# Kernel optimization log

Measured on AMD Instinct MI355X. Metric: run time of the kernel, lower is better.

## Reference

```python
import jax, jax.numpy as jnp
import numpy as np

N_NODES = 100000


def gcn_conv(x, W, b, src, dst, n):
    """PyG GCNConv: linear transform, symmetric-normalized scatter-add, bias.
    src/dst already include self-loops."""
    h = x @ W                                              # [N, out]
    deg = jax.ops.segment_sum(jnp.ones_like(dst, dtype=h.dtype), dst, num_segments=n)
    dinv = jax.lax.rsqrt(deg)                              # deg >= 1 (self-loops)
    norm = dinv[src] * dinv[dst]                           # [E+N]
    msg = h[src] * norm[:, None]                           # gather + scale
    return jax.ops.segment_sum(msg, dst, num_segments=n) + b


def setup_inputs() -> dict:
    key = jax.random.key(0)
    ks = jax.random.split(key, 8)
    N, E = N_NODES, 1600000
    d_in, d_h, d_out = 128, 128, 64
    x = jax.random.normal(ks[0], (N, d_in), dtype=jnp.float32)
    edge_index = jax.random.randint(ks[1], (2, E), 0, N, dtype=jnp.int64)
    W1 = jax.random.normal(ks[2], (d_in, d_h), dtype=jnp.float32) / np.sqrt(d_in)
    b1 = jnp.zeros((d_h,), dtype=jnp.float32)
    W2 = jax.random.normal(ks[3], (d_h, d_out), dtype=jnp.float32) / np.sqrt(d_h)
    b2 = jnp.zeros((d_out,), dtype=jnp.float32)
    Wfc = jax.random.normal(ks[4], (d_out, 10), dtype=jnp.float32) / np.sqrt(d_out)
    bfc = jnp.zeros((10,), dtype=jnp.float32)
    return {"x": x, "edge_index": edge_index, "W1": W1, "b1": b1,
            "W2": W2, "b2": b2, "Wfc": Wfc, "bfc": bfc}


def reference(x, edge_index, W1, b1, W2, b2, Wfc, bfc):
    n = x.shape[0]
    loops = jnp.arange(n, dtype=edge_index.dtype)
    src = jnp.concatenate([edge_index[0], loops])          # add self-loops
    dst = jnp.concatenate([edge_index[1], loops])
    h = jax.nn.relu(gcn_conv(x, W1, b1, src, dst, n))
    h = jax.nn.relu(gcn_conv(h, W2, b2, src, dst, n))
    return h @ Wfc + bfc                                   # [N, 10]
```

## Files before the change

kernel.cpp:

```cpp
#include <hip/hip_runtime.h>
#include <hip/hip_fp16.h>


static constexpr int NB    = 196;
static constexpr int NPB   = 512;
static constexpr int BCAP  = 9216;
static constexpr int CHUNK = 4096;
static constexpr int PARTA = 524;

typedef _Float16 f16x8 __attribute__((ext_vector_type(8)));
typedef float    f32x4 __attribute__((ext_vector_type(4)));

union HV8 { uint4 u; __half2 h2[4]; __half h[8]; };

__device__ inline void acc8(float* a, const HV8& v, float w) {
#pragma unroll
    for (int i = 0; i < 4; ++i) {
        float2 f = __half22float2(v.h2[i]);
        a[2 * i]     = fmaf(f.x, w, a[2 * i]);
        a[2 * i + 1] = fmaf(f.y, w, a[2 * i + 1]);
    }
}

__device__ inline void gemm1_body(int bid, int tid, _Float16 (*Wt)[136],
                                  const float* __restrict__ X,
                                  const float* __restrict__ W,
                                  __half* __restrict__ Hh, int n) {
    for (int idx = tid; idx < 128 * 128; idx += 256) {
        int k = idx >> 7, c = idx & 127;
        Wt[c][k] = (_Float16)W[idx];
    }
    __syncthreads();
    if (bid * 128 >= n) return;

    int wv = tid >> 6, l = tid & 63;
    int lr = l & 15, lq = l >> 4;
    int rowb = bid * 128 + wv * 32;

    f32x4 acc[2][8];
#pragma unroll
    for (int rt = 0; rt < 2; ++rt)
#pragma unroll
        for (int ct = 0; ct < 8; ++ct) acc[rt][ct] = (f32x4){0.f, 0.f, 0.f, 0.f};

#pragma unroll
    for (int kt = 0; kt < 4; ++kt) {
        int kb = kt * 32 + lq * 8;
        f16x8 af[2];
#pragma unroll
        for (int rt = 0; rt < 2; ++rt) {
            int row = rowb + rt * 16 + lr;
            row = (row < n) ? row : (n - 1);
            const float* xr = X + (size_t)row * 128 + kb;
            float4 xa = *(const float4*)xr;
            float4 xb = *(const float4*)(xr + 4);
            f16x8 a;
            a[0] = (_Float16)xa.x; a[1] = (_Float16)xa.y;
            a[2] = (_Float16)xa.z; a[3] = (_Float16)xa.w;
            a[4] = (_Float16)xb.x; a[5] = (_Float16)xb.y;
            a[6] = (_Float16)xb.z; a[7] = (_Float16)xb.w;
            af[rt] = a;
        }
#pragma unroll
        for (int ct = 0; ct < 8; ++ct) {
            f16x8 bf = *(const f16x8*)&Wt[ct * 16 + lr][kb];
            acc[0][ct] = __builtin_amdgcn_mfma_f32_16x16x32_f16(af[0], bf, acc[0][ct], 0, 0, 0);
            acc[1][ct] = __builtin_amdgcn_mfma_f32_16x16x32_f16(af[1], bf, acc[1][ct], 0, 0, 0);
        }
    }
#pragma unroll
    for (int rt = 0; rt < 2; ++rt)
#pragma unroll
        for (int j = 0; j < 4; ++j) {
            int row = rowb + rt * 16 + lq * 4 + j;
            if (row >= n) continue;
            __half* hr = Hh + (size_t)row * 128 + lr;
#pragma unroll
            for (int ct = 0; ct < 8; ++ct)
                hr[ct * 16] = __float2half(acc[rt][ct][j]);
        }
}

union SharedL1 {
    _Float16 Wt[128][136];
    struct {
        int hist[NB]; int lofs[NB]; int gbase[NB]; int lcur[NB]; int scanv[256];
        unsigned pkbuf[CHUNK]; unsigned short bbuf[CHUNK];
    } s;
};

__global__ __launch_bounds__(256) void k_scat_gemm1(
        const int* __restrict__ src, const int* __restrict__ dst, int E,
        int* __restrict__ gcursor, unsigned* __restrict__ ebuf,
        const float* __restrict__ X, const float* __restrict__ W,
        __half* __restrict__ Hh, int n, int nchunks) {
    __shared__ SharedL1 sh;
    int q = blockIdx.x / 7, r = blockIdx.x % 7;
    int tid = threadIdx.x;
    if (r < 3) {
        int fid = q * 3 + r;
        if (fid >= nchunks) return;
        long long e0 = (long long)fid * CHUNK;
        int m = (int)(((long long)E - e0 < CHUNK) ? (E - e0) : CHUNK);

        for (int i = tid; i < NB; i += 256) sh.s.hist[i] = 0;
        __syncthreads();

        unsigned pk[16]; int bk[16];
#pragma unroll
        for (int i = 0; i < 16; ++i) {
            int idx = i * 256 + tid;
            bool ok = idx < m;
            long long e = e0 + idx;
            int d = ok ? dst[e] : 0;
            int s = ok ? src[e] : 0;
            bk[i] = ok ? (d >> 9) : -1;
            pk[i] = ((unsigned)(d & 511) << 17) | (unsigned)s;
            if (ok) atomicAdd(&sh.s.hist[bk[i]], 1);
        }
        __syncthreads();
        int v = (tid < NB) ? sh.s.hist[tid] : 0;
        sh.s.scanv[tid] = v;
        __syncthreads();
        for (int off = 1; off < 256; off <<= 1) {
            int add = (tid >= off) ? sh.s.scanv[tid - off] : 0;
            __syncthreads();
            sh.s.scanv[tid] += add;
            __syncthreads();
        }
        if (tid < NB) {
            int ex = sh.s.scanv[tid] - v;
            sh.s.lofs[tid] = ex;
            sh.s.lcur[tid] = ex;
            sh.s.gbase[tid] = (v > 0) ? atomicAdd(&gcursor[tid], v) : 0;
        }
        __syncthreads();
#pragma unroll
        for (int i = 0; i < 16; ++i) {
            if (bk[i] >= 0) {
                int slot = atomicAdd(&sh.s.lcur[bk[i]], 1);
                sh.s.pkbuf[slot] = pk[i];
                sh.s.bbuf[slot] = (unsigned short)bk[i];
            }
        }
        __syncthreads();
        for (int i = tid; i < m; i += 256) {
            int b = sh.s.bbuf[i];
            int rel = sh.s.gbase[b] + (i - sh.s.lofs[b]);
            if (rel < BCAP) ebuf[(size_t)b * BCAP + rel] = sh.s.pkbuf[i];
        }
        return;
    }
    int bid = q * 4 + (r - 3);
    if (bid >= PARTA) return;
    gemm1_body(bid, tid, sh.Wt, X, W, Hh, n);
}

union SharedL2 {
    _Float16 Wt[128][136];
    struct { int hist[NPB]; int scanv[256]; int rp[NPB]; int reds[256]; } c;
};

__global__ __launch_bounds__(256) void k_csr_gemm1b(
        const unsigned* __restrict__ ebuf, const int* __restrict__ gcursor,
        int* __restrict__ row_ptr, int* __restrict__ col,
        float* __restrict__ dinv, int N_,
        const float* __restrict__ X, const float* __restrict__ W,
        __half* __restrict__ Hh, int n) {
    __shared__ SharedL2 sh;
    int q = blockIdx.x / 7, r = blockIdx.x % 7;
    int tid = threadIdx.x;
    if (r < 3) {
        int b = q * 3 + r;
        if (b >= NB) return;
        int rv = (tid < NB && tid < b) ? min(gcursor[tid], BCAP) : 0;
        sh.c.reds[tid] = rv;
        __syncthreads();
        for (int off = 128; off > 0; off >>= 1) {
            if (tid < off) sh.c.reds[tid] += sh.c.reds[tid + off];
            __syncthreads();
        }
        int base = sh.c.reds[0];
        __syncthreads();

        for (int i = tid; i < NPB; i += 256) sh.c.hist[i] = 0;
        __syncthreads();
        int cntb = min(gcursor[b], BCAP);
        const unsigned* seg = ebuf + (size_t)b * BCAP;
        for (int i = tid; i < cntb; i += 256)
            atomicAdd(&sh.c.hist[seg[i] >> 17], 1);
        __syncthreads();
        int a0 = sh.c.hist[2 * tid], a1 = sh.c.hist[2 * tid + 1];
        int s = a0 + a1;
        sh.c.scanv[tid] = s;
        __syncthreads();
        for (int off = 1; off < 256; off <<= 1) {
            int add = (tid >= off) ? sh.c.scanv[tid - off] : 0;
            __syncthreads();
            sh.c.scanv[tid] += add;
            __syncthreads();
        }
        int excl = sh.c.scanv[tid] - s;
        sh.c.rp[2 * tid] = excl;
        sh.c.rp[2 * tid + 1] = excl + a0;
        __syncthreads();
        int node0 = b * NPB;
        for (int i = tid; i < NPB; i += 256) {
            int node = node0 + i;
            if (node < N_) {
                row_ptr[node] = base + sh.c.rp[i];
                dinv[node] = rsqrtf((float)(sh.c.hist[i] + 1));
            }
        }
        if (tid == 0 && b == NB - 1) row_ptr[N_] = base + cntb;
        __syncthreads();
        for (int i = tid; i < NPB; i += 256) sh.c.rp[i] += base;
        __syncthreads();
        for (int i = tid; i < cntb; i += 256) {
            unsigned pk = seg[i];
            int pos = atomicAdd(&sh.c.rp[pk >> 17], 1);
            col[pos] = (int)(pk & 0x1FFFFu);
        }
        return;
    }
    int bid = PARTA + q * 4 + (r - 3);
    if (bid * 128 >= n) return;
    gemm1_body(bid, tid, sh.Wt, X, W, Hh, n);
}

__global__ __launch_bounds__(256) void k_gather128(const __half* __restrict__ Hs,
                                                   const float* __restrict__ dinv,
                                                   const int* __restrict__ row_ptr,
                                                   const int* __restrict__ col,
                                                   __half* __restrict__ outh, int n) {
    int wave = threadIdx.x >> 6;
    int lane = threadIdx.x & 63;
    int h = lane >> 5, hl = lane & 31;
    int halfbase = h * 32;
    int qi2 = hl >> 4, ql = hl & 15;
    int node = blockIdx.x * 8 + wave * 2 + h;
    if (node >= n) return;
    int beg = row_ptr[node], end = row_ptr[node + 1];
    int deg = end - beg;

    float acc[8];
#pragma unroll
    for (int v = 0; v < 8; ++v) acc[v] = 0.f;

    for (int base = 0; base < deg; base += 32) {
        int m = deg - base; if (m > 32) m = 32;
        int cl = (hl < m) ? col[beg + base + hl] : 0;
        for (int j = 0; j < m; j += 16) {
            int ss[8]; float ww[8]; HV8 uu[8];
#pragma unroll
            for (int t = 0; t < 8; ++t) {
                int jx = j + t * 2 + qi2;
                bool ok = jx < m;
                ss[t] = __shfl(cl, halfbase + (ok ? jx : j));
                ww[t] = ok ? dinv[ss[t]] : 0.f;
            }
#pragma unroll
            for (int t = 0; t < 8; ++t)
                uu[t].u = *(const uint4*)(Hs + (size_t)ss[t] * 128 + ql * 8);
#pragma unroll
            for (int t = 0; t < 8; ++t) acc8(acc, uu[t], ww[t]);
        }
    }
#pragma unroll
    for (int v = 0; v < 8; ++v) acc[v] += __shfl_xor(acc[v], 16);
    if (qi2 == 0) {
        HV8 su; su.u = *(const uint4*)(Hs + (size_t)node * 128 + ql * 8);
        float dn = dinv[node];
        HV8 o;
#pragma unroll
        for (int i = 0; i < 4; ++i) {
            float2 f = __half22float2(su.h2[i]);
            o.h[2 * i]     = __float2half((acc[2 * i]     + dn * f.x) * dn);
            o.h[2 * i + 1] = __float2half((acc[2 * i + 1] + dn * f.y) * dn);
        }
        *(uint4*)(outh + (size_t)node * 128 + ql * 8) = o.u;
    }
}

__global__ __launch_bounds__(256) void k_gemm2(const __half* __restrict__ A,
                                               const float* __restrict__ W2,
                                               const float* __restrict__ b1,
                                               const float* __restrict__ dinv,
                                               __half* __restrict__ Hh2, int n) {
    __shared__ _Float16 Wt[64][136];
    __shared__ _Float16 b1h[128];
    int tid = threadIdx.x;
    for (int idx = tid; idx < 128 * 64; idx += 256) {
        int k = idx >> 6, c = idx & 63;
        Wt[c][k] = (_Float16)W2[idx];
    }
    if (tid < 128) b1h[tid] = (_Float16)b1[tid];
    __syncthreads();

    int bid = blockIdx.x;
    if (bid * 128 >= n) return;
    int wv = tid >> 6, l = tid & 63;
    int lr = l & 15, lq = l >> 4;
    int rowb = bid * 128 + wv * 32;

    f32x4 acc[2][4];
#pragma unroll
    for (int rt = 0; rt < 2; ++rt)
#pragma unroll
        for (int ct = 0; ct < 4; ++ct) acc[rt][ct] = (f32x4){0.f, 0.f, 0.f, 0.f};

#pragma unroll
    for (int kt = 0; kt < 4; ++kt) {
        int kb = kt * 32 + lq * 8;
        f16x8 bb = *(const f16x8*)&b1h[kb];
        f16x8 af[2];
#pragma unroll
        for (int rt = 0; rt < 2; ++rt) {
            int row = rowb + rt * 16 + lr;
            row = (row < n) ? row : (n - 1);
            f16x8 a = *(const f16x8*)(A + (size_t)row * 128 + kb);
            a = a + bb;
#pragma unroll
            for (int i = 0; i < 8; ++i)
                a[i] = (a[i] > (_Float16)0.f) ? a[i] : (_Float16)0.f;
            af[rt] = a;
        }
#pragma unroll
        for (int ct = 0; ct < 4; ++ct) {
            f16x8 bf = *(const f16x8*)&Wt[ct * 16 + lr][kb];
            acc[0][ct] = __builtin_amdgcn_mfma_f32_16x16x32_f16(af[0], bf, acc[0][ct], 0, 0, 0);
            acc[1][ct] = __builtin_amdgcn_mfma_f32_16x16x32_f16(af[1], bf, acc[1][ct], 0, 0, 0);
        }
    }
#pragma unroll
    for (int rt = 0; rt < 2; ++rt)
#pragma unroll
        for (int j = 0; j < 4; ++j) {
            int row = rowb + rt * 16 + lq * 4 + j;
            if (row >= n) continue;
            float dn = dinv[row];
            __half* hr = Hh2 + (size_t)row * 64 + lr;
#pragma unroll
            for (int ct = 0; ct < 4; ++ct)
                hr[ct * 16] = __float2half(acc[rt][ct][j] * dn);
        }
}

__global__ __launch_bounds__(256) void k_gather_fc(const __half* __restrict__ Hs,
                                                   const float* __restrict__ dinv,
                                                   const int* __restrict__ row_ptr,
                                                   const int* __restrict__ col,
                                                   const float* __restrict__ b2,
                                                   const float* __restrict__ Wfc,
                                                   const float* __restrict__ bfc,
                                                   float* __restrict__ out, int n) {
    int wave = threadIdx.x >> 6;
    int lane = threadIdx.x & 63;
    int h = lane >> 5, hl = lane & 31;
    int halfbase = h * 32;
    int oi2 = hl >> 3, ol = hl & 7;
    float wrowA[10], wrowB[10];
#pragma unroll
    for (int j = 0; j < 10; ++j) {
        wrowA[j] = Wfc[(2 * hl) * 10 + j];
        wrowB[j] = Wfc[(2 * hl + 1) * 10 + j];
    }
    float2 b2v = *(const float2*)(b2 + 2 * hl);

    int node = blockIdx.x * 8 + wave * 2 + h;
    if (node >= n) return;
    int beg = row_ptr[node], end = row_ptr[node + 1];
    int deg = end - beg;

    float acc[8];
#pragma unroll
    for (int v = 0; v < 8; ++v) acc[v] = 0.f;

    for (int base = 0; base < deg; base += 32) {
        int m = deg - base; if (m > 32) m = 32;
        int cl = (hl < m) ? col[beg + base + hl] : 0;
        for (int j = 0; j < m; j += 16) {
            int ss[4]; float ww[4]; HV8 uu[4];
#pragma unroll
            for (int t = 0; t < 4; ++t) {
                int jx = j + t * 4 + oi2;
                bool ok = jx < m;
                ss[t] = __shfl(cl, halfbase + (ok ? jx : j));
                ww[t] = ok ? 1.f : 0.f;
            }
#pragma unroll
            for (int t = 0; t < 4; ++t)
                uu[t].u = *(const uint4*)(Hs + (size_t)ss[t] * 64 + ol * 8);
#pragma unroll
            for (int t = 0; t < 4; ++t) acc8(acc, uu[t], ww[t]);
        }
    }
#pragma unroll
    for (int v = 0; v < 8; ++v) {
        acc[v] += __shfl_xor(acc[v], 16);
        acc[v] += __shfl_xor(acc[v], 8);
    }
    int srcl = halfbase + (hl >> 2);
    float vals[8];
#pragma unroll
    for (int v = 0; v < 8; ++v) vals[v] = __shfl(acc[v], srcl);
    int e = (hl & 3) * 2;
    float aggA = vals[0], aggB = vals[1];
#pragma unroll
    for (int v = 2; v < 8; v += 2) {
        aggA = (e == v) ? vals[v] : aggA;
        aggB = (e == v) ? vals[v + 1] : aggB;
    }
    float2 sf = __half22float2(*(const __half2*)(Hs + (size_t)node * 64 + 2 * hl));
    float dn = dinv[node];
    float vA = fmaxf((aggA + sf.x) * dn + b2v.x, 0.f);
    float vB = fmaxf((aggB + sf.y) * dn + b2v.y, 0.f);
    float p[10];
#pragma unroll
    for (int j = 0; j < 10; ++j) p[j] = vA * wrowA[j] + vB * wrowB[j];
#pragma unroll
    for (int off = 16; off > 0; off >>= 1)
#pragma unroll
        for (int j = 0; j < 10; ++j) p[j] += __shfl_xor(p[j], off);
    if (hl == 0) {
        float* o = out + (size_t)node * 10;
#pragma unroll
        for (int j = 0; j < 10; ++j) o[j] = p[j] + bfc[j];
    }
}

static inline int cdiv(long long a, int b) { return (int)((a + b - 1) / b); }

extern "C" void kernel_launch(void* const* d_in, const int* in_sizes, int n_in,
                              void* d_out, int out_size, void* d_ws, size_t ws_size,
                              hipStream_t stream) {
    const float* x   = (const float*)d_in[0];
    const int*   ei  = (const int*)d_in[1];
    const float* W1  = (const float*)d_in[2];
    const float* b1  = (const float*)d_in[3];
    const float* W2  = (const float*)d_in[4];
    const float* b2  = (const float*)d_in[5];
    const float* Wfc = (const float*)d_in[6];
    const float* bfc = (const float*)d_in[7];
    float* out = (float*)d_out;

    const int N = in_sizes[0] / 128;
    const int E = in_sizes[1] / 2;
    const int* src = ei;
    const int* dst = ei + E;

    char* ws = (char*)d_ws;
    size_t off = 0;
    auto alloc = [&](size_t bytes) { void* p = ws + off; off = (off + bytes + 255) & ~(size_t)255; return p; };
    float*    dinv    = (float*)   alloc((size_t)N * 4);
    int*      row_ptr = (int*)     alloc((size_t)(N + 1) * 4);
    int*      gcursor = (int*)     alloc((size_t)NB * 4);
    unsigned* ebuf    = (unsigned*)alloc((size_t)NB * BCAP * 4);
    int*      col     = (int*)     alloc((size_t)E * 4);
    __half*   Hh1     = (__half*)  alloc((size_t)N * 128 * 2);
    __half*   Ah1     = (__half*)  alloc((size_t)N * 128 * 2);
    __half*   Hh2     = (__half*)  alloc((size_t)N * 64 * 2);

    hipMemsetAsync(gcursor, 0, (size_t)NB * 4, stream);

    const int nchunks = cdiv(E, CHUNK);
    const int groupsL1 = max(cdiv(nchunks, 3), cdiv(PARTA, 4));
    k_scat_gemm1<<<groupsL1 * 7, 256, 0, stream>>>(
        src, dst, E, gcursor, ebuf, x, W1, Hh1, N, nchunks);

    const int gemmTotal = cdiv(N, 128);
    const int groupsL2 = max(cdiv(NB, 3), cdiv(gemmTotal - PARTA, 4));
    k_csr_gemm1b<<<groupsL2 * 7, 256, 0, stream>>>(
        ebuf, gcursor, row_ptr, col, dinv, N, x, W1, Hh1, N);

    k_gather128<<<cdiv(N, 8), 256, 0, stream>>>(Hh1, dinv, row_ptr, col, Ah1, N);

    k_gemm2<<<cdiv(N, 128), 256, 0, stream>>>(Ah1, W2, b1, dinv, Hh2, N);
    k_gather_fc<<<cdiv(N, 8), 256, 0, stream>>>(Hh2, dinv, row_ptr, col,
                                                b2, Wfc, bfc, out, N);
}
```

Measured before the change: 270.4 us.

## Fuse layer-1 aggregation into gemm2 via LDS and accumulate gathers in packed fp16

Merges the layer-1 neighbor gather kernel with the second GEMM. Each 128-node block aggregates its rows into a shared-memory tile, then runs the MFMA GEMM from LDS, so the intermediate Ah1 buffer is never written to or read back from global memory. Both gather loops now accumulate in packed fp16 vectors instead of fp32 scalars, which halves the accumulator registers and the reduction shuffles. The risks are reduced occupancy from the roughly 52KB of LDS, only 782 blocks doing serial 16-pass gathers, and lower precision in the fp16 sums.

Measured after the change: 354.5 us. 1.31x slower.

```diff
diff --git a/kernel.cpp b/kernel.cpp
--- a/kernel.cpp
+++ b/kernel.cpp
@@ -10,17 +10,6 @@
 
 typedef _Float16 f16x8 __attribute__((ext_vector_type(8)));
 typedef float    f32x4 __attribute__((ext_vector_type(4)));
-
-union HV8 { uint4 u; __half2 h2[4]; __half h[8]; };
-
-__device__ inline void acc8(float* a, const HV8& v, float w) {
-#pragma unroll
-    for (int i = 0; i < 4; ++i) {
-        float2 f = __half22float2(v.h2[i]);
-        a[2 * i]     = fmaf(f.x, w, a[2 * i]);
-        a[2 * i + 1] = fmaf(f.y, w, a[2 * i + 1]);
-    }
-}
 
 __device__ inline void gemm1_body(int bid, int tid, _Float16 (*Wt)[136],
                                   const float* __restrict__ X,
@@ -228,86 +217,94 @@
     gemm1_body(bid, tid, sh.Wt, X, W, Hh, n);
 }
 
-__global__ __launch_bounds__(256) void k_gather128(const __half* __restrict__ Hs,
-                                                   const float* __restrict__ dinv,
-                                                   const int* __restrict__ row_ptr,
-                                                   const int* __restrict__ col,
-                                                   __half* __restrict__ outh, int n) {
-    int wave = threadIdx.x >> 6;
-    int lane = threadIdx.x & 63;
-    int h = lane >> 5, hl = lane & 31;
-    int halfbase = h * 32;
-    int qi2 = hl >> 4, ql = hl & 15;
-    int node = blockIdx.x * 8 + wave * 2 + h;
-    if (node >= n) return;
-    int beg = row_ptr[node], end = row_ptr[node + 1];
-    int deg = end - beg;
-
-    float acc[8];
-#pragma unroll
-    for (int v = 0; v < 8; ++v) acc[v] = 0.f;
-
-    for (int base = 0; base < deg; base += 32) {
-        int m = deg - base; if (m > 32) m = 32;
-        int cl = (hl < m) ? col[beg + base + hl] : 0;
-        for (int j = 0; j < m; j += 16) {
-            int ss[8]; float ww[8]; HV8 uu[8];
-#pragma unroll
-            for (int t = 0; t < 8; ++t) {
-                int jx = j + t * 2 + qi2;
-                bool ok = jx < m;
-                ss[t] = __shfl(cl, halfbase + (ok ? jx : j));
-                ww[t] = ok ? dinv[ss[t]] : 0.f;
-            }
-#pragma unroll
-            for (int t = 0; t < 8; ++t)
-                uu[t].u = *(const uint4*)(Hs + (size_t)ss[t] * 128 + ql * 8);
-#pragma unroll
-            for (int t = 0; t < 8; ++t) acc8(acc, uu[t], ww[t]);
-        }
-    }
-#pragma unroll
-    for (int v = 0; v < 8; ++v) acc[v] += __shfl_xor(acc[v], 16);
-    if (qi2 == 0) {
-        HV8 su; su.u = *(const uint4*)(Hs + (size_t)node * 128 + ql * 8);
-        float dn = dinv[node];
-        HV8 o;
-#pragma unroll
-        for (int i = 0; i < 4; ++i) {
-            float2 f = __half22float2(su.h2[i]);
-            o.h[2 * i]     = __float2half((acc[2 * i]     + dn * f.x) * dn);
-            o.h[2 * i + 1] = __float2half((acc[2 * i + 1] + dn * f.y) * dn);
-        }
-        *(uint4*)(outh + (size_t)node * 128 + ql * 8) = o.u;
-    }
-}
-
-__global__ __launch_bounds__(256) void k_gemm2(const __half* __restrict__ A,
-                                               const float* __restrict__ W2,
-                                               const float* __restrict__ b1,
-                                               const float* __restrict__ dinv,
-                                               __half* __restrict__ Hh2, int n) {
+__global__ __launch_bounds__(256) void k_agg_gemm2(
+        const __half* __restrict__ Hs, const float* __restrict__ dinv,
+        const int* __restrict__ row_ptr, const int* __restrict__ col,
+        const float* __restrict__ W2, const float* __restrict__ b1,
+        __half* __restrict__ Hh2, int n) {
     __shared__ _Float16 Wt[64][136];
     __shared__ _Float16 b1h[128];
+    __shared__ _Float16 aggB[128][136];
     int tid = threadIdx.x;
     for (int idx = tid; idx < 128 * 64; idx += 256) {
         int k = idx >> 6, c = idx & 63;
         Wt[c][k] = (_Float16)W2[idx];
     }
     if (tid < 128) b1h[tid] = (_Float16)b1[tid];
+
+    int wave = tid >> 6, lane = tid & 63;
+    int h = lane >> 5, hl = lane & 31;
+    int halfbase = h * 32;
+    int qi2 = hl >> 4, ql = hl & 15;
+    int node0 = blockIdx.x * 128;
+
+    for (int p = 0; p < 16; ++p) {
+        int loc = p * 8 + wave * 2 + h;
+        int node = node0 + loc;
+        f16x8 acc;
+#pragma unroll
+        for (int i = 0; i < 8; ++i) acc[i] = (_Float16)0.f;
+        if (node < n) {
+            int beg = row_ptr[node], end = row_ptr[node + 1];
+            int deg = end - beg;
+            for (int base = 0; base < deg; base += 32) {
+                int m = deg - base; if (m > 32) m = 32;
+                int cl = (hl < m) ? col[beg + base + hl] : 0;
+                for (int j = 0; j < m; j += 16) {
+                    int ss[8]; float wf[8];
+#pragma unroll
+                    for (int t = 0; t < 8; ++t) {
+                        int jx = j + t * 2 + qi2;
+                        bool ok = jx < m;
+                        ss[t] = __shfl(cl, halfbase + (ok ? jx : j));
+                        wf[t] = ok ? dinv[ss[t]] : 0.f;
+                    }
+                    f16x8 uu[8];
+#pragma unroll
+                    for (int t = 0; t < 8; ++t)
+                        uu[t] = *(const f16x8*)(Hs + (size_t)ss[t] * 128 + ql * 8);
+#pragma unroll
+                    for (int t = 0; t < 8; ++t) {
+                        _Float16 wh = (_Float16)wf[t];
+                        f16x8 ws;
+#pragma unroll
+                        for (int i = 0; i < 8; ++i) ws[i] = wh;
+                        acc = uu[t] * ws + acc;
+                    }
+                }
+            }
+        }
+        uint4 ai = *(uint4*)&acc;
+        uint4 bi;
+        bi.x = __shfl_xor((int)ai.x, 16); bi.y = __shfl_xor((int)ai.y, 16);
+        bi.z = __shfl_xor((int)ai.z, 16); bi.w = __shfl_xor((int)ai.w, 16);
+        f16x8 other = *(f16x8*)&bi;
+        acc = acc + other;
+        if (qi2 == 0) {
+            f16x8 o;
+            if (node < n) {
+                f16x8 sv = *(const f16x8*)(Hs + (size_t)node * 128 + ql * 8);
+                float dn = dinv[node];
+#pragma unroll
+                for (int i = 0; i < 8; ++i) {
+                    float s = (float)acc[i] + dn * (float)sv[i];
+                    o[i] = (_Float16)(s * dn);
+                }
+            } else {
+#pragma unroll
+                for (int i = 0; i < 8; ++i) o[i] = (_Float16)0.f;
+            }
+            *(f16x8*)&aggB[loc][ql * 8] = o;
+        }
+    }
     __syncthreads();
-
-    int bid = blockIdx.x;
-    if (bid * 128 >= n) return;
-    int wv = tid >> 6, l = tid & 63;
-    int lr = l & 15, lq = l >> 4;
-    int rowb = bid * 128 + wv * 32;
-
-    f32x4 acc[2][4];
+    int lr = lane & 15, lq = lane >> 4;
+    int rowbL = wave * 32;
+    f32x4 acc2[2][4];
 #pragma unroll
     for (int rt = 0; rt < 2; ++rt)
 #pragma unroll
-        for (int ct = 0; ct < 4; ++ct) acc[rt][ct] = (f32x4){0.f, 0.f, 0.f, 0.f};
+        for (int ct = 0; ct < 4; ++ct) acc2[rt][ct] = (f32x4){0.f, 0.f, 0.f, 0.f};
 
 #pragma unroll
     for (int kt = 0; kt < 4; ++kt) {
@@ -316,9 +313,7 @@
         f16x8 af[2];
 #pragma unroll
         for (int rt = 0; rt < 2; ++rt) {
-            int row = rowb + rt * 16 + lr;
-            row = (row < n) ? row : (n - 1);
-            f16x8 a = *(const f16x8*)(A + (size_t)row * 128 + kb);
+            f16x8 a = *(const f16x8*)&aggB[rowbL + rt * 16 + lr][kb];
             a = a + bb;
 #pragma unroll
             for (int i = 0; i < 8; ++i)
@@ -328,21 +323,21 @@
 #pragma unroll
         for (int ct = 0; ct < 4; ++ct) {
             f16x8 bf = *(const f16x8*)&Wt[ct * 16 + lr][kb];
-            acc[0][ct] = __builtin_amdgcn_mfma_f32_16x16x32_f16(af[0], bf, acc[0][ct], 0, 0, 0);
-            acc[1][ct] = __builtin_amdgcn_mfma_f32_16x16x32_f16(af[1], bf, acc[1][ct], 0, 0, 0);
+            acc2[0][ct] = __builtin_amdgcn_mfma_f32_16x16x32_f16(af[0], bf, acc2[0][ct], 0, 0, 0);
+            acc2[1][ct] = __builtin_amdgcn_mfma_f32_16x16x32_f16(af[1], bf, acc2[1][ct], 0, 0, 0);
         }
     }
 #pragma unroll
     for (int rt = 0; rt < 2; ++rt)
 #pragma unroll
         for (int j = 0; j < 4; ++j) {
-            int row = rowb + rt * 16 + lq * 4 + j;
+            int row = node0 + rowbL + rt * 16 + lq * 4 + j;
             if (row >= n) continue;
             float dn = dinv[row];
             __half* hr = Hh2 + (size_t)row * 64 + lr;
 #pragma unroll
             for (int ct = 0; ct < 4; ++ct)
-                hr[ct * 16] = __float2half(acc[rt][ct][j] * dn);
+                hr[ct * 16] = __float2half(acc2[rt][ct][j] * dn);
         }
 }
 
@@ -372,49 +367,63 @@
     int beg = row_ptr[node], end = row_ptr[node + 1];
     int deg = end - beg;
 
-    float acc[8];
-#pragma unroll
-    for (int v = 0; v < 8; ++v) acc[v] = 0.f;
+    f16x8 acc;
+#pragma unroll
+    for (int i = 0; i < 8; ++i) acc[i] = (_Float16)0.f;
 
     for (int base = 0; base < deg; base += 32) {
         int m = deg - base; if (m > 32) m = 32;
         int cl = (hl < m) ? col[beg + base + hl] : 0;
         for (int j = 0; j < m; j += 16) {
-            int ss[4]; float ww[4]; HV8 uu[4];
+            int ss[4]; float wf[4];
 #pragma unroll
             for (int t = 0; t < 4; ++t) {
                 int jx = j + t * 4 + oi2;
                 bool ok = jx < m;
                 ss[t] = __shfl(cl, halfbase + (ok ? jx : j));
-                ww[t] = ok ? 1.f : 0.f;
-            }
+                wf[t] = ok ? 1.f : 0.f;
+            }
+            f16x8 uu[4];
 #pragma unroll
             for (int t = 0; t < 4; ++t)
-                uu[t].u = *(const uint4*)(Hs + (size_t)ss[t] * 64 + ol * 8);
-#pragma unroll
-            for (int t = 0; t < 4; ++t) acc8(acc, uu[t], ww[t]);
-        }
-    }
-#pragma unroll
-    for (int v = 0; v < 8; ++v) {
-        acc[v] += __shfl_xor(acc[v], 16);
-        acc[v] += __shfl_xor(acc[v], 8);
-    }
+                uu[t] = *(const f16x8*)(Hs + (size_t)ss[t] * 64 + ol * 8);
+#pragma unroll
+            for (int t = 0; t < 4; ++t) {
+                _Float16 wh = (_Float16)wf[t];
+                f16x8 ws;
+#pragma unroll
+                for (int i = 0; i < 8; ++i) ws[i] = wh;
+                acc = uu[t] * ws + acc;
+            }
+        }
+    }
+#pragma unroll
+    for (int off = 16; off >= 8; off >>= 1) {
+        uint4 ai = *(uint4*)&acc;
+        uint4 bi;
+        bi.x = __shfl_xor((int)ai.x, off); bi.y = __shfl_xor((int)ai.y, off);
+        bi.z = __shfl_xor((int)ai.z, off); bi.w = __shfl_xor((int)ai.w, off);
+        f16x8 other = *(f16x8*)&bi;
+        acc = acc + other;
+    }
+    float av[8];
+#pragma unroll
+    for (int v = 0; v < 8; ++v) av[v] = (float)acc[v];
     int srcl = halfbase + (hl >> 2);
     float vals[8];
 #pragma unroll
-    for (int v = 0; v < 8; ++v) vals[v] = __shfl(acc[v], srcl);
+    for (int v = 0; v < 8; ++v) vals[v] = __shfl(av[v], srcl);
     int e = (hl & 3) * 2;
-    float aggA = vals[0], aggB = vals[1];
+    float aggA = vals[0], aggB2 = vals[1];
 #pragma unroll
     for (int v = 2; v < 8; v += 2) {
         aggA = (e == v) ? vals[v] : aggA;
-        aggB = (e == v) ? vals[v + 1] : aggB;
+        aggB2 = (e == v) ? vals[v + 1] : aggB2;
     }
     float2 sf = __half22float2(*(const __half2*)(Hs + (size_t)node * 64 + 2 * hl));
     float dn = dinv[node];
     float vA = fmaxf((aggA + sf.x) * dn + b2v.x, 0.f);
-    float vB = fmaxf((aggB + sf.y) * dn + b2v.y, 0.f);
+    float vB = fmaxf((aggB2 + sf.y) * dn + b2v.y, 0.f);
     float p[10];
 #pragma unroll
     for (int j = 0; j < 10; ++j) p[j] = vA * wrowA[j] + vB * wrowB[j];
@@ -458,7 +467,6 @@
     unsigned* ebuf    = (unsigned*)alloc((size_t)NB * BCAP * 4);
     int*      col     = (int*)     alloc((size_t)E * 4);
     __half*   Hh1     = (__half*)  alloc((size_t)N * 128 * 2);
-    __half*   Ah1     = (__half*)  alloc((size_t)N * 128 * 2);
     __half*   Hh2     = (__half*)  alloc((size_t)N * 64 * 2);
 
     hipMemsetAsync(gcursor, 0, (size_t)NB * 4, stream);
@@ -473,9 +481,9 @@
     k_csr_gemm1b<<<groupsL2 * 7, 256, 0, stream>>>(
         ebuf, gcursor, row_ptr, col, dinv, N, x, W1, Hh1, N);
 
-    k_gather128<<<cdiv(N, 8), 256, 0, stream>>>(Hh1, dinv, row_ptr, col, Ah1, N);
-
-    k_gemm2<<<cdiv(N, 128), 256, 0, stream>>>(Ah1, W2, b1, dinv, Hh2, N);
+    k_agg_gemm2<<<cdiv(N, 128), 256, 0, stream>>>(Hh1, dinv, row_ptr, col,
+                                                  W2, b1, Hh2, N);
+
     k_gather_fc<<<cdiv(N, 8), 256, 0, stream>>>(Hh2, dinv, row_ptr, col,
                                                 b2, Wfc, bfc, out, N);
 }
```
